# Optimization experiments

Hardware: AMD Instinct MI355X
Metric: run time of the kernel (lower is better)

## Reference

```python
import jax, jax.numpy as jnp
import numpy as np

EPS = 1e-5          # module's self.eps
CLAMP = 1e-8        # numerical floor for norms
MAX_EUCLID = 32.0   # rescale_to_max_euclid cap (best-effort reconstruction)


def _linner(u, v):
    # Lorentz inner product <u,v>_L = -u0*v0 + <u_s,v_s>, keepdims on last axis
    uv = jnp.sum(u * v, axis=-1, keepdims=True)
    return uv - 2.0 * u[..., :1] * v[..., :1]


def _centroid(x):
    # Lorentzian (weighted) centroid: mean then renormalize onto hyperboloid (k=1)
    avg = jnp.mean(x, axis=-2)
    denom = jnp.sqrt(jnp.clip(-_linner(avg, avg), CLAMP, None))
    return avg / denom


def _logmap(x, y):
    # log_x(y) on Lorentz model, k=1
    alpha = jnp.clip(-_linner(x, y), 1.0 + 1e-7, None)
    u = y - alpha * x
    unorm = jnp.sqrt(jnp.clip(_linner(u, u), CLAMP, None))
    return jnp.arccosh(alpha) * u / unorm


def _plus_origin(y):
    # y + o where o = (1, 0, ..., 0)
    return jnp.concatenate([y[..., :1] + 1.0, y[..., 1:]], axis=-1)


def _transp0back(y, v):
    # parallel transport T_{y->o}(v): v + <o,v>_L/(1 - <y,o>_L) * (y + o); <o,v>_L = -v0
    coef = -v[..., :1] / (1.0 + y[..., :1])
    return v + coef * _plus_origin(y)


def _transp0(y, v):
    # parallel transport T_{o->y}(v): v + <y,v>_L/(1 + y0) * (o + y)
    coef = _linner(y, v) / (1.0 + y[..., :1])
    return v + coef * _plus_origin(y)


def _expmap(x, u):
    # exp_x(u) on Lorentz model, k=1
    nu = jnp.sqrt(jnp.clip(_linner(u, u), CLAMP, None))
    return jnp.cosh(nu) * x + jnp.sinh(nu) * u / nu


def _rescale_to_max_euclid(x):
    n = jnp.sqrt(jnp.sum(x * x, axis=-1, keepdims=True))
    return x * jnp.minimum(1.0, MAX_EUCLID / jnp.maximum(n, CLAMP))


def setup_inputs() -> dict:
    key = jax.random.key(0)
    B, S, D = 64, 4096, 128
    raw = 0.5 * jax.random.normal(key, (B, S, D - 1), dtype=jnp.float32)
    time = jnp.sqrt(1.0 + jnp.sum(raw * raw, axis=-1, keepdims=True))
    x = jnp.concatenate([time, raw], axis=-1)  # points on the hyperboloid
    gamma = jnp.ones((D,), dtype=jnp.float32)
    beta = jnp.zeros((D,), dtype=jnp.float32).at[0].set(1.0)  # manifold origin
    return {"x": x, "gamma": gamma, "beta": beta}


def reference(x, gamma, beta):
    # Training-mode Lorentz batchnorm (3D input path)
    mean = _centroid(x)       # (B, D)
    mean = _centroid(mean)    # (D,)
    x_T = _logmap(mean, x)            # tangent vectors at mean, (B, S, D)
    x_T = _transp0back(mean, x_T)     # transport to tangent space at origin
    var = jnp.sqrt(jnp.var(x_T, axis=(0, 1)) + EPS)   # Frechet per-feature std, (D,)
    x_T = x_T * (gamma / (var + EPS))
    x_T = _rescale_to_max_euclid(x_T)
    x_T = _transp0(beta, x_T)         # transport to tangent space at beta
    return _expmap(beta, x_T)
```

## Files before the change

kernel.cpp:

```cpp
#include <hip/hip_runtime.h>
#include <math.h>

#define NB 64
#define NS 4096
#define ND 128
#define NPTS (NB * NS)
#define PPB 256
#define NBLK (NPTS / PPB)
#define EPSV 1e-5f
#define CLAMPV 1e-8f
#define MAXEUC 32.0f

__device__ __forceinline__ float rcp_f(float x) { return __builtin_amdgcn_rcpf(x); }
__device__ __forceinline__ float rsq_f(float x) { return __builtin_amdgcn_rsqf(x); }

__device__ __forceinline__ float hred(float v) {
#pragma unroll
    for (int o = 16; o > 0; o >>= 1) v += __shfl_xor(v, o, 64);
    return v;
}

__global__ __launch_bounds__(256) void k1(const float4* __restrict__ x4,
                                          float4* __restrict__ part1) {
    const int b = blockIdx.x >> 3;
    const int c = blockIdx.x & 7;
    const int d4 = threadIdx.x & 31;
    const int g  = threadIdx.x >> 5;
    const int srow = c * 512 + g;
    const float4* p = x4 + ((long long)b * NS + srow) * 32 + d4;
    float4 acc = make_float4(0.f, 0.f, 0.f, 0.f);
#pragma unroll 4
    for (int i = 0; i < 64; ++i) {
        float4 v = p[(long long)i * 8 * 32];
        acc.x += v.x; acc.y += v.y; acc.z += v.z; acc.w += v.w;
    }
    __shared__ float4 red[256];
    red[threadIdx.x] = acc;
    __syncthreads();
    if (threadIdx.x < 32) {
        float4 r = red[threadIdx.x];
#pragma unroll
        for (int gg = 1; gg < 8; ++gg) {
            float4 v = red[gg * 32 + threadIdx.x];
            r.x += v.x; r.y += v.y; r.z += v.z; r.w += v.w;
        }
        part1[(long long)blockIdx.x * 32 + threadIdx.x] = r;
    }
}

__global__ __launch_bounds__(1024) void k2(const float* __restrict__ part1,
                                           float* __restrict__ meanG) {
    __shared__ float avgL[NB * ND];
    __shared__ float avg2L[ND];
    __shared__ float denomS;
    const int t = threadIdx.x;
    for (int idx = t; idx < NB * ND; idx += 1024) {
        int b = idx >> 7, d = idx & 127;
        float s = 0.f;
#pragma unroll
        for (int c = 0; c < 8; ++c) s += part1[((b << 3) + c) * ND + d];
        avgL[idx] = s * (1.0f / (float)NS);
    }
    __syncthreads();
    const int w = t >> 6, l = t & 63;
    for (int b = w; b < NB; b += 16) {
        float a0 = avgL[b * ND + l];
        float a1 = avgL[b * ND + 64 + l];
        float a00 = avgL[b * ND];
        float s = a0 * a0 + a1 * a1;
#pragma unroll
        for (int o = 32; o > 0; o >>= 1) s += __shfl_xor(s, o, 64);
        float denom = sqrtf(fmaxf(2.f * a00 * a00 - s, CLAMPV));
        avgL[b * ND + l] = a0 / denom;
        avgL[b * ND + 64 + l] = a1 / denom;
    }
    __syncthreads();
    if (t < ND) {
        float s = 0.f;
        for (int b = 0; b < NB; ++b) s += avgL[b * ND + t];
        avg2L[t] = s * (1.0f / (float)NB);
    }
    __syncthreads();
    if (w == 0) {
        float a0 = avg2L[l], a1 = avg2L[l + 64];
        float s = a0 * a0 + a1 * a1;
#pragma unroll
        for (int o = 32; o > 0; o >>= 1) s += __shfl_xor(s, o, 64);
        float a00 = avg2L[0];
        float denom = sqrtf(fmaxf(2.f * a00 * a00 - s, CLAMPV));
        if (l == 0) denomS = denom;
    }
    __syncthreads();
    if (t < ND) meanG[t] = avg2L[t] / denomS;
}

__device__ __forceinline__ void point_scalars(const float4& xv, const float4& m,
                                              float m0, float inv1pm0, int l,
                                              float& fac, float& hcoef) {
    float dot = xv.x * m.x + xv.y * m.y + xv.z * m.z + xv.w * m.w;
    dot = hred(dot);
    float x0 = __shfl(xv.x, l & 32, 64);
    float alpha = fmaxf(2.f * m0 * x0 - dot, 1.0f + 1e-7f);
    float am1 = alpha * alpha - 1.f;
    float sq = sqrtf(fmaxf(am1, CLAMPV));
    fac = __logf(alpha + sq) * rcp_f(sq);
    float u0 = x0 - alpha * m0;
    hcoef = -fac * (alpha + u0 * inv1pm0);
}

__global__ __launch_bounds__(256) void k3(const float4* __restrict__ x4,
                                          const float* __restrict__ meanG,
                                          float* __restrict__ part3) {
    const int l = threadIdx.x & 63;
    const int w = threadIdx.x >> 6;
    const int h = l >> 5;
    const int fl = l & 31;
    const float4 m = ((const float4*)meanG)[fl];
    const float m0 = meanG[0];
    const float inv1pm0 = rcp_f(1.f + m0);
    float4 s = make_float4(0.f, 0.f, 0.f, 0.f);
    float4 q = make_float4(0.f, 0.f, 0.f, 0.f);
    const long long base = (long long)blockIdx.x * PPB;
#pragma unroll 4
    for (int i = 0; i < PPB / 8; ++i) {
        long long p = base + (long long)i * 8 + (w << 1) + h;
        float4 xv = x4[p * 32 + fl];
        float fac, hc;
        point_scalars(xv, m, m0, inv1pm0, l, fac, hc);
        float t0 = fac * xv.x + hc * m.x;
        float t1 = fac * xv.y + hc * m.y;
        float t2 = fac * xv.z + hc * m.z;
        float t3 = fac * xv.w + hc * m.w;
        if (fl == 0) t0 = 0.f;
        s.x += t0; s.y += t1; s.z += t2; s.w += t3;
        q.x += t0 * t0; q.y += t1 * t1; q.z += t2 * t2; q.w += t3 * t3;
    }
    __shared__ float4 ls[8][32];
    __shared__ float4 lq[8][32];
    const int copy = (w << 1) + h;
    ls[copy][fl] = s;
    lq[copy][fl] = q;
    __syncthreads();
    if (threadIdx.x < ND) {
        int d = threadIdx.x;
        const float* lsf = (const float*)ls;
        const float* lqf = (const float*)lq;
        float S = 0.f, Q = 0.f;
#pragma unroll
        for (int cc = 0; cc < 8; ++cc) { S += lsf[cc * ND + d]; Q += lqf[cc * ND + d]; }
        part3[blockIdx.x * (2 * ND) + d] = S;
        part3[blockIdx.x * (2 * ND) + ND + d] = Q;
    }
}

__global__ __launch_bounds__(1024) void k4(const float* __restrict__ part3,
                                           const float* __restrict__ gamma,
                                           float* __restrict__ scaleG) {
    const int t = threadIdx.x;
    const int d = t & 127, g = t >> 7;
    double S = 0.0, Q = 0.0;
    for (int b = g; b < NBLK; b += 8) {
        S += (double)part3[b * (2 * ND) + d];
        Q += (double)part3[b * (2 * ND) + ND + d];
    }
    __shared__ double sS[8][ND];
    __shared__ double sQ[8][ND];
    sS[g][d] = S; sQ[g][d] = Q;
    __syncthreads();
    if (t < ND) {
        double St = 0.0, Qt = 0.0;
#pragma unroll
        for (int gg = 0; gg < 8; ++gg) { St += sS[gg][d]; Qt += sQ[gg][d]; }
        const double N = (double)NPTS;
        double mu = St / N;
        double var = Qt / N - mu * mu;
        if (var < 0.0) var = 0.0;
        float stdv = sqrtf((float)var + EPSV);
        scaleG[d] = gamma[d] / (stdv + EPSV);
    }
}

__global__ __launch_bounds__(256) void k5(const float4* __restrict__ x4,
                                          const float* __restrict__ meanG,
                                          const float* __restrict__ scaleG,
                                          const float* __restrict__ betaG,
                                          float4* __restrict__ out4) {
    const int l = threadIdx.x & 63;
    const int w = threadIdx.x >> 6;
    const int h = l >> 5;
    const int fl = l & 31;
    const float4 m  = ((const float4*)meanG)[fl];
    const float4 sc = ((const float4*)scaleG)[fl];
    const float4 bt = ((const float4*)betaG)[fl];
    const float m0 = meanG[0];
    const float b0 = betaG[0];
    const float inv1pm0 = rcp_f(1.f + m0);
    const float inv1pb0 = rcp_f(1.f + b0);
    const long long base = (long long)blockIdx.x * PPB;
#pragma unroll 4
    for (int i = 0; i < PPB / 8; ++i) {
        long long p = base + (long long)i * 8 + (w << 1) + h;
        float4 xv = x4[p * 32 + fl];
        float fac, hc;
        point_scalars(xv, m, m0, inv1pm0, l, fac, hc);
        float ts0 = sc.x * (fac * xv.x + hc * m.x);
        float ts1 = sc.y * (fac * xv.y + hc * m.y);
        float ts2 = sc.z * (fac * xv.z + hc * m.z);
        float ts3 = sc.w * (fac * xv.w + hc * m.w);
        if (fl == 0) ts0 = 0.f;
        float nn = ts0 * ts0 + ts1 * ts1 + ts2 * ts2 + ts3 * ts3;
        float bd = bt.x * ts0 + bt.y * ts1 + bt.z * ts2 + bt.w * ts3;
#pragma unroll
        for (int o = 16; o > 0; o >>= 1) {
            nn += __shfl_xor(nn, o, 64);
            bd += __shfl_xor(bd, o, 64);
        }
        float n = sqrtf(nn);
        float r = fminf(1.f, MAXEUC * rcp_f(fmaxf(n, CLAMPV)));
        float coef2 = r * bd * inv1pb0;
        float nu2 = r * n; nu2 *= nu2;
        float nu = sqrtf(fmaxf(nu2, CLAMPV));
        float e = __expf(nu);
        float ei = rcp_f(e);
        float ch = 0.5f * (e + ei);
        float sf = (0.5f * (e - ei)) * rcp_f(nu);
        float A = ch + sf * coef2;
        float Bc = sf * r;
        float o0 = Bc * ts0 + A * bt.x;
        float o1 = Bc * ts1 + A * bt.y;
        float o2 = Bc * ts2 + A * bt.z;
        float o3 = Bc * ts3 + A * bt.w;
        if (fl == 0) o0 += sf * coef2;
        out4[p * 32 + fl] = make_float4(o0, o1, o2, o3);
    }
}

extern "C" void kernel_launch(void* const* d_in, const int* in_sizes, int n_in,
                              void* d_out, int out_size, void* d_ws, size_t ws_size,
                              hipStream_t stream) {
    const float* x = (const float*)d_in[0];
    const float* gamma = (const float*)d_in[1];
    const float* beta = (const float*)d_in[2];
    float* out = (float*)d_out;
    float* ws = (float*)d_ws;

    float* part1  = ws;
    float* meanG  = ws + 65536;
    float* scaleG = ws + 65536 + 128;
    float* part3  = ws + 65536 + 256;

    k1<<<NB * 8, 256, 0, stream>>>((const float4*)x, (float4*)part1);
    k2<<<1, 1024, 0, stream>>>(part1, meanG);
    k3<<<NBLK, 256, 0, stream>>>((const float4*)x, meanG, part3);
    k4<<<1, 1024, 0, stream>>>(part3, gamma, scaleG);
    k5<<<NBLK, 256, 0, stream>>>((const float4*)x, meanG, scaleG, beta, (float4*)out);
}
```

Baseline: 324.9 us.

## Map each point to 16 lanes with two float4s and DPP row reductions

Restructures k3 and k5 so each point is handled by a 16-lane row, with each lane holding two float4 chunks, in place of 32 lanes holding one. The per-point dot-product and norm reductions now use DPP row operations in place of cross-lane shuffles. The Lorentz inner product is folded into a pre-signed weight vector, so the separate x0 broadcast and its shuffle go away. The intent is to cut the shuffle/LDS traffic and reduction latency of these memory-bound passes. In exchange each lane keeps more registers live, and the nu clamp changes slightly (1e-4 instead of the sqrt of 1e-8).

```diff
diff --git a/kernel.cpp b/kernel.cpp
--- a/kernel.cpp
+++ b/kernel.cpp
@@ -12,11 +12,16 @@
 #define MAXEUC 32.0f
 
 __device__ __forceinline__ float rcp_f(float x) { return __builtin_amdgcn_rcpf(x); }
-__device__ __forceinline__ float rsq_f(float x) { return __builtin_amdgcn_rsqf(x); }
-
-__device__ __forceinline__ float hred(float v) {
-#pragma unroll
-    for (int o = 16; o > 0; o >>= 1) v += __shfl_xor(v, o, 64);
+
+#define DPP_ADD(v, ctrl)                                                            \
+    v += __int_as_float(__builtin_amdgcn_update_dpp(0, __float_as_int(v), (ctrl),   \
+                                                    0xF, 0xF, true))
+
+__device__ __forceinline__ float row16_sum(float v) {
+    DPP_ADD(v, 0x128);
+    DPP_ADD(v, 0x124);
+    DPP_ADD(v, 0x122);
+    DPP_ADD(v, 0x121);
     return v;
 }
 
@@ -94,60 +99,72 @@
     if (t < ND) meanG[t] = avg2L[t] / denomS;
 }
 
-__device__ __forceinline__ void point_scalars(const float4& xv, const float4& m,
-                                              float m0, float inv1pm0, int l,
-                                              float& fac, float& hcoef) {
-    float dot = xv.x * m.x + xv.y * m.y + xv.z * m.z + xv.w * m.w;
-    dot = hred(dot);
-    float x0 = __shfl(xv.x, l & 32, 64);
-    float alpha = fmaxf(2.f * m0 * x0 - dot, 1.0f + 1e-7f);
+__device__ __forceinline__ void point_scalars16(const float4& xa, const float4& xb,
+                                                const float4& wa, const float4& wb,
+                                                float m0, float inv1pm0, int fl,
+                                                float& fac, float& hcoef) {
+    float ad = wa.x * xa.x + wa.y * xa.y + wa.z * xa.z + wa.w * xa.w
+             + wb.x * xb.x + wb.y * xb.y + wb.z * xb.z + wb.w * xb.w;
+    float px = (fl == 0) ? xa.x : 0.f;
+    ad = row16_sum(ad);
+    px = row16_sum(px);
+    float alpha = fmaxf(ad, 1.0f + 1e-7f);
     float am1 = alpha * alpha - 1.f;
     float sq = sqrtf(fmaxf(am1, CLAMPV));
     fac = __logf(alpha + sq) * rcp_f(sq);
-    float u0 = x0 - alpha * m0;
-    hcoef = -fac * (alpha + u0 * inv1pm0);
+    hcoef = -fac * (alpha + px) * inv1pm0;
 }
 
 __global__ __launch_bounds__(256) void k3(const float4* __restrict__ x4,
                                           const float* __restrict__ meanG,
                                           float* __restrict__ part3) {
-    const int l = threadIdx.x & 63;
-    const int w = threadIdx.x >> 6;
-    const int h = l >> 5;
-    const int fl = l & 31;
-    const float4 m = ((const float4*)meanG)[fl];
+    const int fl = threadIdx.x & 15;
+    const int pg = threadIdx.x >> 4;
+    const float4* m4 = (const float4*)meanG;
+    const float4 ma = m4[fl], mb = m4[fl + 16];
     const float m0 = meanG[0];
     const float inv1pm0 = rcp_f(1.f + m0);
-    float4 s = make_float4(0.f, 0.f, 0.f, 0.f);
-    float4 q = make_float4(0.f, 0.f, 0.f, 0.f);
+    float4 wa = make_float4(-ma.x, -ma.y, -ma.z, -ma.w);
+    float4 wb = make_float4(-mb.x, -mb.y, -mb.z, -mb.w);
+    if (fl == 0) wa.x = ma.x;
+    float4 sa = make_float4(0.f, 0.f, 0.f, 0.f), sb = sa, qa = sa, qb = sa;
     const long long base = (long long)blockIdx.x * PPB;
 #pragma unroll 4
-    for (int i = 0; i < PPB / 8; ++i) {
-        long long p = base + (long long)i * 8 + (w << 1) + h;
-        float4 xv = x4[p * 32 + fl];
+    for (int i = 0; i < PPB / 16; ++i) {
+        long long p = base + (long long)i * 16 + pg;
+        float4 xa = x4[p * 32 + fl];
+        float4 xb = x4[p * 32 + fl + 16];
         float fac, hc;
-        point_scalars(xv, m, m0, inv1pm0, l, fac, hc);
-        float t0 = fac * xv.x + hc * m.x;
-        float t1 = fac * xv.y + hc * m.y;
-        float t2 = fac * xv.z + hc * m.z;
-        float t3 = fac * xv.w + hc * m.w;
+        point_scalars16(xa, xb, wa, wb, m0, inv1pm0, fl, fac, hc);
+        float t0 = fac * xa.x + hc * ma.x;
+        float t1 = fac * xa.y + hc * ma.y;
+        float t2 = fac * xa.z + hc * ma.z;
+        float t3 = fac * xa.w + hc * ma.w;
+        float t4 = fac * xb.x + hc * mb.x;
+        float t5 = fac * xb.y + hc * mb.y;
+        float t6 = fac * xb.z + hc * mb.z;
+        float t7 = fac * xb.w + hc * mb.w;
         if (fl == 0) t0 = 0.f;
-        s.x += t0; s.y += t1; s.z += t2; s.w += t3;
-        q.x += t0 * t0; q.y += t1 * t1; q.z += t2 * t2; q.w += t3 * t3;
-    }
-    __shared__ float4 ls[8][32];
-    __shared__ float4 lq[8][32];
-    const int copy = (w << 1) + h;
-    ls[copy][fl] = s;
-    lq[copy][fl] = q;
+        sa.x += t0; sa.y += t1; sa.z += t2; sa.w += t3;
+        sb.x += t4; sb.y += t5; sb.z += t6; sb.w += t7;
+        qa.x += t0 * t0; qa.y += t1 * t1; qa.z += t2 * t2; qa.w += t3 * t3;
+        qb.x += t4 * t4; qb.y += t5 * t5; qb.z += t6 * t6; qb.w += t7 * t7;
+    }
+    __shared__ float ls[16][ND];
+    __shared__ float lq[16][ND];
+    float* ps = &ls[pg][fl * 8];
+    float* pq = &lq[pg][fl * 8];
+    ps[0] = sa.x; ps[1] = sa.y; ps[2] = sa.z; ps[3] = sa.w;
+    ps[4] = sb.x; ps[5] = sb.y; ps[6] = sb.z; ps[7] = sb.w;
+    pq[0] = qa.x; pq[1] = qa.y; pq[2] = qa.z; pq[3] = qa.w;
+    pq[4] = qb.x; pq[5] = qb.y; pq[6] = qb.z; pq[7] = qb.w;
     __syncthreads();
     if (threadIdx.x < ND) {
         int d = threadIdx.x;
-        const float* lsf = (const float*)ls;
-        const float* lqf = (const float*)lq;
+        int slot = ((d & 63) >> 2) * 8 + (d >> 6) * 4 + (d & 3);
         float S = 0.f, Q = 0.f;
 #pragma unroll
-        for (int cc = 0; cc < 8; ++cc) { S += lsf[cc * ND + d]; Q += lqf[cc * ND + d]; }
+        for (int cc = 0; cc < 16; ++cc) { S += ls[cc][slot]; Q += lq[cc][slot]; }
         part3[blockIdx.x * (2 * ND) + d] = S;
         part3[blockIdx.x * (2 * ND) + ND + d] = Q;
     }
@@ -185,53 +202,66 @@
                                           const float* __restrict__ scaleG,
                                           const float* __restrict__ betaG,
                                           float4* __restrict__ out4) {
-    const int l = threadIdx.x & 63;
-    const int w = threadIdx.x >> 6;
-    const int h = l >> 5;
-    const int fl = l & 31;
-    const float4 m  = ((const float4*)meanG)[fl];
-    const float4 sc = ((const float4*)scaleG)[fl];
-    const float4 bt = ((const float4*)betaG)[fl];
+    const int fl = threadIdx.x & 15;
+    const int pg = threadIdx.x >> 4;
+    const float4* m4 = (const float4*)meanG;
+    const float4* s4 = (const float4*)scaleG;
+    const float4* b4 = (const float4*)betaG;
+    const float4 ma = m4[fl], mb = m4[fl + 16];
+    const float4 sca = s4[fl], scb = s4[fl + 16];
+    const float4 bta = b4[fl], btb = b4[fl + 16];
     const float m0 = meanG[0];
     const float b0 = betaG[0];
     const float inv1pm0 = rcp_f(1.f + m0);
     const float inv1pb0 = rcp_f(1.f + b0);
+    float4 wa = make_float4(-ma.x, -ma.y, -ma.z, -ma.w);
+    float4 wb = make_float4(-mb.x, -mb.y, -mb.z, -mb.w);
+    if (fl == 0) wa.x = ma.x;
     const long long base = (long long)blockIdx.x * PPB;
 #pragma unroll 4
-    for (int i = 0; i < PPB / 8; ++i) {
-        long long p = base + (long long)i * 8 + (w << 1) + h;
-        float4 xv = x4[p * 32 + fl];
+    for (int i = 0; i < PPB / 16; ++i) {
+        long long p = base + (long long)i * 16 + pg;
+        float4 xa = x4[p * 32 + fl];
+        float4 xb = x4[p * 32 + fl + 16];
         float fac, hc;
-        point_scalars(xv, m, m0, inv1pm0, l, fac, hc);
-        float ts0 = sc.x * (fac * xv.x + hc * m.x);
-        float ts1 = sc.y * (fac * xv.y + hc * m.y);
-        float ts2 = sc.z * (fac * xv.z + hc * m.z);
-        float ts3 = sc.w * (fac * xv.w + hc * m.w);
+        point_scalars16(xa, xb, wa, wb, m0, inv1pm0, fl, fac, hc);
+        float ts0 = sca.x * (fac * xa.x + hc * ma.x);
+        float ts1 = sca.y * (fac * xa.y + hc * ma.y);
+        float ts2 = sca.z * (fac * xa.z + hc * ma.z);
+        float ts3 = sca.w * (fac * xa.w + hc * ma.w);
+        float ts4 = scb.x * (fac * xb.x + hc * mb.x);
+        float ts5 = scb.y * (fac * xb.y + hc * mb.y);
+        float ts6 = scb.z * (fac * xb.z + hc * mb.z);
+        float ts7 = scb.w * (fac * xb.w + hc * mb.w);
         if (fl == 0) ts0 = 0.f;
-        float nn = ts0 * ts0 + ts1 * ts1 + ts2 * ts2 + ts3 * ts3;
-        float bd = bt.x * ts0 + bt.y * ts1 + bt.z * ts2 + bt.w * ts3;
-#pragma unroll
-        for (int o = 16; o > 0; o >>= 1) {
-            nn += __shfl_xor(nn, o, 64);
-            bd += __shfl_xor(bd, o, 64);
-        }
+        float nn = ts0 * ts0 + ts1 * ts1 + ts2 * ts2 + ts3 * ts3
+                 + ts4 * ts4 + ts5 * ts5 + ts6 * ts6 + ts7 * ts7;
+        float bd = bta.x * ts0 + bta.y * ts1 + bta.z * ts2 + bta.w * ts3
+                 + btb.x * ts4 + btb.y * ts5 + btb.z * ts6 + btb.w * ts7;
+        nn = row16_sum(nn);
+        bd = row16_sum(bd);
         float n = sqrtf(nn);
         float r = fminf(1.f, MAXEUC * rcp_f(fmaxf(n, CLAMPV)));
         float coef2 = r * bd * inv1pb0;
-        float nu2 = r * n; nu2 *= nu2;
-        float nu = sqrtf(fmaxf(nu2, CLAMPV));
+        float nu = fmaxf(r * n, 1e-4f);
         float e = __expf(nu);
         float ei = rcp_f(e);
         float ch = 0.5f * (e + ei);
         float sf = (0.5f * (e - ei)) * rcp_f(nu);
         float A = ch + sf * coef2;
         float Bc = sf * r;
-        float o0 = Bc * ts0 + A * bt.x;
-        float o1 = Bc * ts1 + A * bt.y;
-        float o2 = Bc * ts2 + A * bt.z;
-        float o3 = Bc * ts3 + A * bt.w;
-        if (fl == 0) o0 += sf * coef2;
-        out4[p * 32 + fl] = make_float4(o0, o1, o2, o3);
+        float4 oa, ob;
+        oa.x = Bc * ts0 + A * bta.x;
+        oa.y = Bc * ts1 + A * bta.y;
+        oa.z = Bc * ts2 + A * bta.z;
+        oa.w = Bc * ts3 + A * bta.w;
+        ob.x = Bc * ts4 + A * btb.x;
+        ob.y = Bc * ts5 + A * btb.y;
+        ob.z = Bc * ts6 + A * btb.z;
+        ob.w = Bc * ts7 + A * btb.w;
+        if (fl == 0) oa.x += sf * coef2;
+        out4[p * 32 + fl] = oa;
+        out4[p * 32 + fl + 16] = ob;
     }
 }
 
```

New measurement: 319.9 us. About the same (-1.5%).
